# Optimization experiments

Measured on AMD Instinct MI355X. Metric: run time of the kernel, lower is better.

The kernel has to match this reference:

```python
import jax, jax.numpy as jnp
import numpy as np

NEG_BIG = -1e38

def setup_inputs() -> dict:
    key = jax.random.key(0)
    kq, kk, kv, kwq, kwk = jax.random.split(key, 5)
    B, S, d_model, d_k, d_v = 4, 4096, 256, 64, 64
    return {
        "q": jax.random.normal(kq, (B, S, d_model), dtype=jnp.float32),
        "k": jax.random.normal(kk, (B, S, d_model), dtype=jnp.float32),
        "v": jax.random.normal(kv, (B, S, d_v), dtype=jnp.float32),
        "w_q": jax.random.normal(kwq, (d_k, d_model), dtype=jnp.float32) * 0.01,
        "w_k": jax.random.normal(kwk, (d_k, d_model), dtype=jnp.float32) * 0.01,
    }

def reference(q, k, v, w_q, w_k):
    d_k = w_q.shape[0]
    temperature = jnp.asarray(np.power(d_k, 0.5), dtype=q.dtype)
    # relu-projected Q, K: [B,S,d_k]
    qp = jax.nn.relu(jnp.einsum("bsm,km->bsk", q, w_q))
    kp = jax.nn.relu(jnp.einsum("bsm,km->bsk", k, w_k))
    # scores [B,S,S]
    attn = jnp.einsum("bqd,bkd->bqk", qp, kp) / temperature
    # force column 0 to -1e38 (inline custom mask)
    attn = attn.at[:, :, 0].set(NEG_BIG)
    attn = jax.nn.softmax(attn, axis=2)
    # dropout is identity in eval / p=0
    out = jnp.einsum("bqk,bkd->bqd", attn, v)
    return out
```

## Files before the change

kernel.cpp:

```cpp
#include <hip/hip_runtime.h>

#define B_    4
#define S_    4096
#define DM    256
#define DK    64
#define NROWS (B_ * S_)
#define LOG2E 1.4426950408889634f
#define PACK_BIAS 0.0028151295f

typedef __attribute__((ext_vector_type(8))) short bfrag;
typedef __attribute__((ext_vector_type(4))) float ffrag;

__device__ __forceinline__ unsigned bf16_rne_hi(float x) {
    unsigned u = __float_as_uint(x);
    return u + 0x7fffu + ((u >> 16) & 1u);
}
__device__ __forceinline__ unsigned short f2bf(float x) {
    return (unsigned short)(bf16_rne_hi(x) >> 16);
}
__device__ __forceinline__ unsigned pack_bf16x2(float lo, float hi) {
    return (bf16_rne_hi(hi) & 0xffff0000u) | (bf16_rne_hi(lo) >> 16);
}

__device__ __forceinline__ float fast_exp2(float x) {
#if __has_builtin(__builtin_amdgcn_exp2f)
    return __builtin_amdgcn_exp2f(x);
#else
    float r;
    asm("v_exp_f32 %0, %1\n\ts_nop 1" : "=v"(r) : "v"(x));
    return r;
#endif
}

__device__ __forceinline__ unsigned trunc_pack_bf16x2(float lo, float hi) {
    return __builtin_amdgcn_perm(__float_as_uint(hi), __float_as_uint(lo),
                                 0x07060302u);
}

__global__ __launch_bounds__(256) void fused_prep(
    const float* __restrict__ q, const float* __restrict__ k,
    const float* __restrict__ v, const float* __restrict__ wq,
    const float* __restrict__ wk, unsigned short* __restrict__ vT,
    unsigned short* __restrict__ qpb, unsigned short* __restrict__ kpb)
{
    __shared__ __align__(16) char smem[64 * 264 * 2];
    const int blk  = blockIdx.x;
    const int lane = threadIdx.x & 63, w = threadIdx.x >> 6;

    if (blk < 256) {
        float (*tile)[65] = (float(*)[65])smem;
        const int b = blk >> 6, s0 = (blk & 63) * 64;
#pragma unroll
        for (int i = 0; i < 16; ++i) {
            const int sl = i * 4 + w;
            tile[sl][lane] = v[(b * S_ + s0 + sl) * DK + lane];
        }
        __syncthreads();
        const int t32 = lane >> 5, pos = lane & 31;
        const int keyl = t32 * 32 + ((pos & 1) ? (pos >> 1) + 16 : (pos >> 1));
#pragma unroll
        for (int i = 0; i < 16; ++i) {
            const int d = i * 4 + w;
            vT[((size_t)(b * 128 + (s0 >> 5) + t32) * 64 + d) * 32 + pos] =
                f2bf(tile[keyl][d]);
        }
    } else {
        unsigned short* wlds = (unsigned short*)smem;
        const int pb = blk - 256;
        const int half = pb >> 8, rblk = pb & 255;
        const float* x;
        const float* wsrc;
        unsigned short* o;
        float scale;
        if (half == 0) { x = q; wsrc = wq; o = qpb; scale = 0.125f * LOG2E; }
        else           { x = k; wsrc = wk; o = kpb; scale = 1.0f; }

#pragma unroll
        for (int i = 0; i < 16; ++i) {
            const int idx4 = i * 256 + threadIdx.x;
            const int r = idx4 >> 6, c4 = idx4 & 63;
            const float4 wv = ((const float4*)wsrc)[idx4];
            uint2 pk;
            pk.x = pack_bf16x2(wv.x, wv.y);
            pk.y = pack_bf16x2(wv.z, wv.w);
            *(uint2*)&wlds[r * 264 + c4 * 4] = pk;
        }
        __syncthreads();

        const int m = lane & 15, quad = lane >> 4;
        const int rows0 = rblk * 64 + w * 16;
        const float* xrow = x + (size_t)(rows0 + m) * DM + quad * 8;

        ffrag acc[4];
#pragma unroll
        for (int dt = 0; dt < 4; ++dt) acc[dt] = (ffrag)(0.0f);

        float4 xb[2][2];
        xb[0][0] = ((const float4*)xrow)[0];
        xb[0][1] = ((const float4*)xrow)[1];

#pragma unroll 2
        for (int kf = 0; kf < 8; ++kf) {
            const int p = kf & 1;
            if (kf < 7) {
                const float4* xn = (const float4*)(xrow + (kf + 1) * 32);
                xb[p ^ 1][0] = xn[0];
                xb[p ^ 1][1] = xn[1];
            }
            union { bfrag v; unsigned u[4]; } pk;
            pk.u[0] = pack_bf16x2(xb[p][0].x, xb[p][0].y);
            pk.u[1] = pack_bf16x2(xb[p][0].z, xb[p][0].w);
            pk.u[2] = pack_bf16x2(xb[p][1].x, xb[p][1].y);
            pk.u[3] = pack_bf16x2(xb[p][1].z, xb[p][1].w);
#pragma unroll
            for (int dt = 0; dt < 4; ++dt) {
                const bfrag Bf = *(const bfrag*)&wlds[(dt * 16 + m) * 264 + kf * 32 + quad * 8];
                acc[dt] = __builtin_amdgcn_mfma_f32_16x16x32_bf16(pk.v, Bf, acc[dt], 0, 0, 0);
            }
        }
#pragma unroll
        for (int dt = 0; dt < 4; ++dt)
#pragma unroll
            for (int r = 0; r < 4; ++r)
                o[(rows0 + quad * 4 + r) * DK + dt * 16 + m] =
                    f2bf(fmaxf(acc[dt][r], 0.0f) * scale);
    }
}

__global__ __launch_bounds__(256) void attn_mfma(
    const unsigned short* __restrict__ qp, const unsigned short* __restrict__ kp,
    const unsigned short* __restrict__ vT, float* __restrict__ num_part,
    float* __restrict__ den_part)
{
    __shared__ __align__(16) char smem[20480];
    unsigned short* Plds = (unsigned short*)smem;
    float* red0 = (float*)smem;
    float* red1 = (float*)smem + 2560;

    const int lane = threadIdx.x & 63, w = threadIdx.x >> 6;
    const int m = lane & 15, quad = lane >> 4;
    const int qg = blockIdx.x;
    const int qbase = qg * 32;
    const int b = qg >> 7;
    const int kstart = (blockIdx.y * 4 + w) * 512;

    bfrag qa[2][2];
#pragma unroll
    for (int mt = 0; mt < 2; ++mt)
#pragma unroll
        for (int kf = 0; kf < 2; ++kf)
            qa[mt][kf] = *(const bfrag*)&qp[(qbase + mt * 16 + m) * DK + kf * 32 + quad * 8];

    ffrag oacc[2][4];
    float dacc[2][4];
#pragma unroll
    for (int mt = 0; mt < 2; ++mt) {
#pragma unroll
        for (int dt = 0; dt < 4; ++dt) oacc[mt][dt] = (ffrag)(0.0f);
#pragma unroll
        for (int r = 0; r < 4; ++r) dacc[mt][r] = 0.0f;
    }

    const unsigned short* kptr = kp + ((size_t)b * S_ + kstart + m) * DK + quad * 8;
    const unsigned short* vptr = vT + ((size_t)(b * 128 + (kstart >> 5)) * 64 + m) * 32 + quad * 8;
    unsigned short* Pw = Plds + w * 1280;

    const ffrag cbias = (ffrag)(PACK_BIAS);

    bfrag kbuf[2][2][2], vbuf[2][4];
#pragma unroll
    for (int kt = 0; kt < 2; ++kt)
#pragma unroll
        for (int kf = 0; kf < 2; ++kf)
            kbuf[0][kt][kf] = *(const bfrag*)(kptr + kt * 1024 + kf * 32);
#pragma unroll
    for (int dt = 0; dt < 4; ++dt)
        vbuf[0][dt] = *(const bfrag*)(vptr + dt * 512);

    bfrag pa0, pa1;

#pragma unroll 2
    for (int jj = 0; jj < 16; ++jj) {
        const int p = jj & 1;

        if (jj < 15) {
            const unsigned short* kn = kptr + (jj + 1) * 2048;
#pragma unroll
            for (int kt = 0; kt < 2; ++kt)
#pragma unroll
                for (int kf = 0; kf < 2; ++kf)
                    kbuf[p ^ 1][kt][kf] = *(const bfrag*)(kn + kt * 1024 + kf * 32);
        }

        if (jj > 0) {
#pragma unroll
            for (int dt = 0; dt < 4; ++dt) {
                oacc[0][dt] = __builtin_amdgcn_mfma_f32_16x16x32_bf16(pa0, vbuf[p ^ 1][dt], oacc[0][dt], 0, 0, 0);
                oacc[1][dt] = __builtin_amdgcn_mfma_f32_16x16x32_bf16(pa1, vbuf[p ^ 1][dt], oacc[1][dt], 0, 0, 0);
            }
        }

        if (jj < 15) {
            const unsigned short* vn = vptr + (jj + 1) * 2048;
#pragma unroll
            for (int dt = 0; dt < 4; ++dt)
                vbuf[p ^ 1][dt] = *(const bfrag*)(vn + dt * 512);
        }

        ffrag s[2][2];
#pragma unroll
        for (int mt = 0; mt < 2; ++mt)
#pragma unroll
            for (int kt = 0; kt < 2; ++kt) {
                ffrag t = __builtin_amdgcn_mfma_f32_16x16x32_bf16(qa[mt][0], kbuf[p][kt][0], cbias, 0, 0, 0);
                s[mt][kt] = __builtin_amdgcn_mfma_f32_16x16x32_bf16(qa[mt][1], kbuf[p][kt][1], t, 0, 0, 0);
            }

        const bool mask0 = (jj == 0) && (kstart == 0) && (m == 0);
#pragma unroll
        for (int mt = 0; mt < 2; ++mt)
#pragma unroll
            for (int r = 0; r < 4; ++r) {
                float e0 = fast_exp2(s[mt][0][r]);
                float e1 = fast_exp2(s[mt][1][r]);
                if (mask0) e0 = 0.0f;
                dacc[mt][r] += e0 + e1;
                *(unsigned*)&Pw[(mt * 16 + quad * 4 + r) * 40 + m * 2] =
                    trunc_pack_bf16x2(e0, e1);
            }

        pa0 = *(const bfrag*)&Pw[(m) * 40 + quad * 8];
        pa1 = *(const bfrag*)&Pw[(16 + m) * 40 + quad * 8];
    }
#pragma unroll
    for (int dt = 0; dt < 4; ++dt) {
        oacc[0][dt] = __builtin_amdgcn_mfma_f32_16x16x32_bf16(pa0, vbuf[1][dt], oacc[0][dt], 0, 0, 0);
        oacc[1][dt] = __builtin_amdgcn_mfma_f32_16x16x32_bf16(pa1, vbuf[1][dt], oacc[1][dt], 0, 0, 0);
    }

#pragma unroll
    for (int mt = 0; mt < 2; ++mt)
#pragma unroll
        for (int r = 0; r < 4; ++r) {
            float d = dacc[mt][r];
            d += __shfl_xor(d, 1, 64);
            d += __shfl_xor(d, 2, 64);
            d += __shfl_xor(d, 4, 64);
            d += __shfl_xor(d, 8, 64);
            dacc[mt][r] = d;
        }

    __syncthreads();
    float* red[2] = { red0, red1 };
    if (w >= 2) {
#pragma unroll
        for (int mt = 0; mt < 2; ++mt) {
#pragma unroll
            for (int dt = 0; dt < 4; ++dt)
#pragma unroll
                for (int r = 0; r < 4; ++r)
                    red[w - 2][((mt * 4 + dt) * 4 + r) * 64 + lane] = oacc[mt][dt][r];
#pragma unroll
            for (int r = 0; r < 4; ++r)
                red[w - 2][2048 + (mt * 4 + r) * 64 + lane] = dacc[mt][r];
        }
    }
    __syncthreads();
    if (w < 2) {
#pragma unroll
        for (int mt = 0; mt < 2; ++mt) {
#pragma unroll
            for (int dt = 0; dt < 4; ++dt)
#pragma unroll
                for (int r = 0; r < 4; ++r)
                    oacc[mt][dt][r] += red[w][((mt * 4 + dt) * 4 + r) * 64 + lane];
#pragma unroll
            for (int r = 0; r < 4; ++r)
                dacc[mt][r] += red[w][2048 + (mt * 4 + r) * 64 + lane];
        }
    }
    __syncthreads();
    if (w == 1) {
#pragma unroll
        for (int mt = 0; mt < 2; ++mt) {
#pragma unroll
            for (int dt = 0; dt < 4; ++dt)
#pragma unroll
                for (int r = 0; r < 4; ++r)
                    red0[((mt * 4 + dt) * 4 + r) * 64 + lane] = oacc[mt][dt][r];
#pragma unroll
            for (int r = 0; r < 4; ++r)
                red0[2048 + (mt * 4 + r) * 64 + lane] = dacc[mt][r];
        }
    }
    __syncthreads();
    if (w == 0) {
        const int gy = blockIdx.y;
#pragma unroll
        for (int mt = 0; mt < 2; ++mt) {
#pragma unroll
            for (int dt = 0; dt < 4; ++dt)
#pragma unroll
                for (int r = 0; r < 4; ++r) {
                    const float nv = oacc[mt][dt][r] + red0[((mt * 4 + dt) * 4 + r) * 64 + lane];
                    num_part[(size_t)gy * NROWS * DK +
                             (qbase + mt * 16 + quad * 4 + r) * DK + dt * 16 + m] = nv;
                }
#pragma unroll
            for (int r = 0; r < 4; ++r) {
                const float dv = dacc[mt][r] + red0[2048 + (mt * 4 + r) * 64 + lane];
                if (m == 0)
                    den_part[gy * NROWS + qbase + mt * 16 + quad * 4 + r] = dv;
            }
        }
    }
}

__global__ __launch_bounds__(256) void finalize_kernel(
    const float* __restrict__ num_part, const float* __restrict__ den_part,
    float* __restrict__ out)
{
    const int i4 = blockIdx.x * 256 + threadIdx.x;
    const int row = i4 >> 4;
    const float4 a = ((const float4*)num_part)[i4];
    const float4 c = ((const float4*)(num_part + (size_t)NROWS * DK))[i4];
    const float inv = 1.0f / (den_part[row] + den_part[NROWS + row]);
    float4 o;
    o.x = (a.x + c.x) * inv;
    o.y = (a.y + c.y) * inv;
    o.z = (a.z + c.z) * inv;
    o.w = (a.w + c.w) * inv;
    ((float4*)out)[i4] = o;
}

extern "C" void kernel_launch(void* const* d_in, const int* in_sizes, int n_in,
                              void* d_out, int out_size, void* d_ws, size_t ws_size,
                              hipStream_t stream)
{
    const float* q  = (const float*)d_in[0];
    const float* k  = (const float*)d_in[1];
    const float* v  = (const float*)d_in[2];
    const float* wq = (const float*)d_in[3];
    const float* wk = (const float*)d_in[4];
    float* out = (float*)d_out;

    char* p = (char*)d_ws;
    unsigned short* qpb = (unsigned short*)p;   p += (size_t)NROWS * DK * 2;
    unsigned short* kpb = (unsigned short*)p;   p += (size_t)NROWS * DK * 2;
    unsigned short* vT  = (unsigned short*)p;   p += (size_t)B_ * DK * S_ * 2;
    float* num_part     = (float*)p;            p += (size_t)2 * NROWS * DK * 4;
    float* den_part     = (float*)p;

    fused_prep<<<768, 256, 0, stream>>>(q, k, v, wq, wk, vT, qpb, kpb);
    attn_mfma<<<dim3(512, 2), 256, 0, stream>>>(qpb, kpb, vT, num_part, den_part);
    finalize_kernel<<<NROWS * DK / 4 / 256, 256, 0, stream>>>(num_part, den_part, out);
}
```

Before: 135.8 us.

## Split attention keys four ways, remap blocks, and restage prep through LDS

The attention kernel now splits the key range into four parts instead of two. Each wave covers 256 keys over 8 iterations, and the grid is a flat 2048 blocks whose index puts the 16 batch/split combinations in the low bits so neighbouring blocks share K/V data. The finalize kernel sums four partials. In the prep kernel, x is staged as bf16 in LDS while the weights are read from global memory and converted per fragment, and the V transpose now uses float4 loads with packed bf16x2 stores. The aim is more parallelism and better cache locality, paid for with more partial-sum traffic and repeated weight loads.

```diff
diff --git a/kernel.cpp b/kernel.cpp
--- a/kernel.cpp
+++ b/kernel.cpp
@@ -7,6 +7,8 @@
 #define NROWS (B_ * S_)
 #define LOG2E 1.4426950408889634f
 #define PACK_BIAS 0.0028151295f
+#define NSPLIT 4
+#define NJ     8
 
 typedef __attribute__((ext_vector_type(8))) short bfrag;
 typedef __attribute__((ext_vector_type(4))) float ffrag;
@@ -43,29 +45,36 @@
     const float* __restrict__ wk, unsigned short* __restrict__ vT,
     unsigned short* __restrict__ qpb, unsigned short* __restrict__ kpb)
 {
-    __shared__ __align__(16) char smem[64 * 264 * 2];
+    __shared__ __align__(16) char smem[64 * 260 * 2];
     const int blk  = blockIdx.x;
     const int lane = threadIdx.x & 63, w = threadIdx.x >> 6;
 
     if (blk < 256) {
         float (*tile)[65] = (float(*)[65])smem;
         const int b = blk >> 6, s0 = (blk & 63) * 64;
-#pragma unroll
-        for (int i = 0; i < 16; ++i) {
-            const int sl = i * 4 + w;
-            tile[sl][lane] = v[(b * S_ + s0 + sl) * DK + lane];
+        const float4* src = (const float4*)(v + (size_t)(b * S_ + s0) * DK);
+#pragma unroll
+        for (int i = 0; i < 4; ++i) {
+            const int idx4 = i * 256 + threadIdx.x;
+            const int row = idx4 >> 4, c4 = idx4 & 15;
+            const float4 vv = src[idx4];
+            tile[row][c4 * 4 + 0] = vv.x;
+            tile[row][c4 * 4 + 1] = vv.y;
+            tile[row][c4 * 4 + 2] = vv.z;
+            tile[row][c4 * 4 + 3] = vv.w;
         }
         __syncthreads();
-        const int t32 = lane >> 5, pos = lane & 31;
-        const int keyl = t32 * 32 + ((pos & 1) ? (pos >> 1) + 16 : (pos >> 1));
-#pragma unroll
-        for (int i = 0; i < 16; ++i) {
-            const int d = i * 4 + w;
-            vT[((size_t)(b * 128 + (s0 >> 5) + t32) * 64 + d) * 32 + pos] =
-                f2bf(tile[keyl][d]);
+        unsigned* dst = (unsigned*)(vT + (size_t)(b * 128 + (s0 >> 5)) * 64 * 32);
+#pragma unroll
+        for (int i = 0; i < 8; ++i) {
+            const int u = i * 256 + threadIdx.x;
+            const int t32 = u >> 10, rem = u & 1023;
+            const int d = rem >> 4, c = rem & 15;
+            dst[(t32 * 64 + d) * 16 + c] =
+                pack_bf16x2(tile[t32 * 32 + c][d], tile[t32 * 32 + c + 16][d]);
         }
     } else {
-        unsigned short* wlds = (unsigned short*)smem;
+        unsigned short* xlds = (unsigned short*)smem;
         const int pb = blk - 256;
         const int half = pb >> 8, rblk = pb & 255;
         const float* x;
@@ -75,47 +84,40 @@
         if (half == 0) { x = q; wsrc = wq; o = qpb; scale = 0.125f * LOG2E; }
         else           { x = k; wsrc = wk; o = kpb; scale = 1.0f; }
 
+        const size_t rows_blk = (size_t)rblk * 64;
+        const float4* xsrc = (const float4*)(x + rows_blk * DM);
 #pragma unroll
         for (int i = 0; i < 16; ++i) {
             const int idx4 = i * 256 + threadIdx.x;
-            const int r = idx4 >> 6, c4 = idx4 & 63;
-            const float4 wv = ((const float4*)wsrc)[idx4];
-            uint2 pk;
-            pk.x = pack_bf16x2(wv.x, wv.y);
-            pk.y = pack_bf16x2(wv.z, wv.w);
-            *(uint2*)&wlds[r * 264 + c4 * 4] = pk;
+            const int row = idx4 >> 6, c4 = idx4 & 63;
+            const float4 xv = xsrc[idx4];
+            uint2 pk2;
+            pk2.x = pack_bf16x2(xv.x, xv.y);
+            pk2.y = pack_bf16x2(xv.z, xv.w);
+            *(uint2*)&xlds[row * 260 + c4 * 4] = pk2;
         }
         __syncthreads();
 
         const int m = lane & 15, quad = lane >> 4;
-        const int rows0 = rblk * 64 + w * 16;
-        const float* xrow = x + (size_t)(rows0 + m) * DM + quad * 8;
+        const int rows0 = (int)rows_blk + w * 16;
 
         ffrag acc[4];
 #pragma unroll
         for (int dt = 0; dt < 4; ++dt) acc[dt] = (ffrag)(0.0f);
 
-        float4 xb[2][2];
-        xb[0][0] = ((const float4*)xrow)[0];
-        xb[0][1] = ((const float4*)xrow)[1];
-
-#pragma unroll 2
+#pragma unroll
         for (int kf = 0; kf < 8; ++kf) {
-            const int p = kf & 1;
-            if (kf < 7) {
-                const float4* xn = (const float4*)(xrow + (kf + 1) * 32);
-                xb[p ^ 1][0] = xn[0];
-                xb[p ^ 1][1] = xn[1];
-            }
-            union { bfrag v; unsigned u[4]; } pk;
-            pk.u[0] = pack_bf16x2(xb[p][0].x, xb[p][0].y);
-            pk.u[1] = pack_bf16x2(xb[p][0].z, xb[p][0].w);
-            pk.u[2] = pack_bf16x2(xb[p][1].x, xb[p][1].y);
-            pk.u[3] = pack_bf16x2(xb[p][1].z, xb[p][1].w);
+            const bfrag A = *(const bfrag*)&xlds[(w * 16 + m) * 260 + kf * 32 + quad * 8];
 #pragma unroll
             for (int dt = 0; dt < 4; ++dt) {
-                const bfrag Bf = *(const bfrag*)&wlds[(dt * 16 + m) * 264 + kf * 32 + quad * 8];
-                acc[dt] = __builtin_amdgcn_mfma_f32_16x16x32_bf16(pk.v, Bf, acc[dt], 0, 0, 0);
+                const float4* wr = (const float4*)&wsrc[(dt * 16 + m) * DM + kf * 32 + quad * 8];
+                const float4 w0 = wr[0], w1 = wr[1];
+                union { bfrag v; unsigned u[4]; } bk;
+                bk.u[0] = pack_bf16x2(w0.x, w0.y);
+                bk.u[1] = pack_bf16x2(w0.z, w0.w);
+                bk.u[2] = pack_bf16x2(w1.x, w1.y);
+                bk.u[3] = pack_bf16x2(w1.z, w1.w);
+                acc[dt] = __builtin_amdgcn_mfma_f32_16x16x32_bf16(A, bk.v, acc[dt], 0, 0, 0);
             }
         }
 #pragma unroll
@@ -139,10 +141,11 @@
 
     const int lane = threadIdx.x & 63, w = threadIdx.x >> 6;
     const int m = lane & 15, quad = lane >> 4;
-    const int qg = blockIdx.x;
-    const int qbase = qg * 32;
-    const int b = qg >> 7;
-    const int kstart = (blockIdx.y * 4 + w) * 512;
+    const int sid = blockIdx.x & 15;
+    const int b   = sid >> 2, gy = sid & 3;
+    const int qgw = blockIdx.x >> 4;
+    const int qbase = (b * 128 + qgw) * 32;
+    const int kstart = (gy * 4 + w) * 256;
 
     bfrag qa[2][2];
 #pragma unroll
@@ -180,10 +183,10 @@
     bfrag pa0, pa1;
 
 #pragma unroll 2
-    for (int jj = 0; jj < 16; ++jj) {
+    for (int jj = 0; jj < NJ; ++jj) {
         const int p = jj & 1;
 
-        if (jj < 15) {
+        if (jj < NJ - 1) {
             const unsigned short* kn = kptr + (jj + 1) * 2048;
 #pragma unroll
             for (int kt = 0; kt < 2; ++kt)
@@ -200,7 +203,7 @@
             }
         }
 
-        if (jj < 15) {
+        if (jj < NJ - 1) {
             const unsigned short* vn = vptr + (jj + 1) * 2048;
 #pragma unroll
             for (int dt = 0; dt < 4; ++dt)
@@ -295,7 +298,6 @@
     }
     __syncthreads();
     if (w == 0) {
-        const int gy = blockIdx.y;
 #pragma unroll
         for (int mt = 0; mt < 2; ++mt) {
 #pragma unroll
@@ -322,14 +324,20 @@
 {
     const int i4 = blockIdx.x * 256 + threadIdx.x;
     const int row = i4 >> 4;
-    const float4 a = ((const float4*)num_part)[i4];
-    const float4 c = ((const float4*)(num_part + (size_t)NROWS * DK))[i4];
-    const float inv = 1.0f / (den_part[row] + den_part[NROWS + row]);
+    float4 n = ((const float4*)num_part)[i4];
+    float d = den_part[row];
+#pragma unroll
+    for (int p = 1; p < NSPLIT; ++p) {
+        const float4 a = ((const float4*)(num_part + (size_t)p * NROWS * DK))[i4];
+        n.x += a.x; n.y += a.y; n.z += a.z; n.w += a.w;
+        d += den_part[p * NROWS + row];
+    }
+    const float inv = 1.0f / d;
     float4 o;
-    o.x = (a.x + c.x) * inv;
-    o.y = (a.y + c.y) * inv;
-    o.z = (a.z + c.z) * inv;
-    o.w = (a.w + c.w) * inv;
+    o.x = n.x * inv;
+    o.y = n.y * inv;
+    o.z = n.z * inv;
+    o.w = n.w * inv;
     ((float4*)out)[i4] = o;
 }
 
@@ -348,10 +356,10 @@
     unsigned short* qpb = (unsigned short*)p;   p += (size_t)NROWS * DK * 2;
     unsigned short* kpb = (unsigned short*)p;   p += (size_t)NROWS * DK * 2;
     unsigned short* vT  = (unsigned short*)p;   p += (size_t)B_ * DK * S_ * 2;
-    float* num_part     = (float*)p;            p += (size_t)2 * NROWS * DK * 4;
+    float* num_part     = (float*)p;            p += (size_t)NSPLIT * NROWS * DK * 4;
     float* den_part     = (float*)p;
 
     fused_prep<<<768, 256, 0, stream>>>(q, k, v, wq, wk, vT, qpb, kpb);
-    attn_mfma<<<dim3(512, 2), 256, 0, stream>>>(qpb, kpb, vT, num_part, den_part);
+    attn_mfma<<<2048, 256, 0, stream>>>(qpb, kpb, vT, num_part, den_part);
     finalize_kernel<<<NROWS * DK / 4 / 256, 256, 0, stream>>>(num_part, den_part, out);
 }
```

Result: slower. 153.7 us (+13.2%).
